# Kernel tuning notes

Measured on AMD Instinct MI355X. Metric: run time of the kernel, lower is better.

The kernel has to match this reference:

```python
import jax, jax.numpy as jnp
import numpy as np

B, N, D, H, E = 4, 4096, 1024, 16, 256
HD = D // H  # head_dim = 64


def setup_inputs() -> dict:
    key = jax.random.key(0)
    k1, k2, k3, k4, k5 = jax.random.split(key, 5)
    scale = 1.0 / np.sqrt(D)
    return {
        "x": jax.random.normal(k1, (B, N, D), dtype=jnp.float32),
        "proj_weight_all": jax.random.normal(k2, (N, E), dtype=jnp.float32) * (1.0 / np.sqrt(N)),
        "W_q": jax.random.normal(k3, (D, D), dtype=jnp.float32) * scale,
        "W_k": jax.random.normal(k4, (D, D), dtype=jnp.float32) * scale,
        "W_v": jax.random.normal(k5, (D, D), dtype=jnp.float32) * scale,
    }


def reference(x, proj_weight_all, W_q, W_k, W_v):
    # QKV projections: [B,N,D] @ [D,D] -> [B,N,D]
    q = jnp.einsum('bnd,de->bne', x, W_q)
    k = jnp.einsum('bnd,de->bne', x, W_k)
    v = jnp.einsum('bnd,de->bne', x, W_v)
    # split heads -> [B,H,N,hd]
    split = lambda t: t.reshape(B, N, H, HD).transpose(0, 2, 1, 3)
    qh, kh, vh = split(q), split(k), split(v)
    # low-rank sequence projection of K/V: [B,H,N,hd] x [N,E] -> [B,H,E,hd]
    k_proj = jnp.einsum('bhnd,ne->bhed', kh, proj_weight_all)
    v_proj = jnp.einsum('bhnd,ne->bhed', vh, proj_weight_all)
    # attention over projected length E (dropout p=0 -> identity)
    scores = jnp.einsum('bhnd,bhed->bhne', qh, k_proj) / jnp.sqrt(jnp.float32(HD))
    attn = jax.nn.softmax(scores, axis=-1)  # [B,H,N,E]
    out = jnp.einsum('bhne,bhed->bhnd', attn, v_proj)
    # concat heads -> [B,N,D]
    return out.transpose(0, 2, 1, 3).reshape(B, N, D)
```

## Files before the change

kernel.cpp:

```cpp
#include <hip/hip_runtime.h>
#include <hip/hip_bf16.h>

#define B_ 4
#define N_ 4096
#define D_ 1024
#define H_ 16
#define E_ 256
#define HD_ 64

typedef __attribute__((ext_vector_type(8))) short bf16x8;
typedef __attribute__((ext_vector_type(4))) short shortx4;
typedef __attribute__((ext_vector_type(4))) float floatx4;

__device__ inline short f2bf(float f) {
  __hip_bfloat16 h = __float2bfloat16(f);
  short s;
  __builtin_memcpy(&s, &h, 2);
  return s;
}

__device__ inline void gld_lds16(const short* g, short* l) {
  __builtin_amdgcn_global_load_lds(
      (const __attribute__((address_space(1))) void*)g,
      (__attribute__((address_space(3))) void*)l, 16, 0, 0);
}

template <bool CAST_COPY>
__device__ inline void transpose_body(const float* __restrict__ src,
                                      short* __restrict__ dstT,
                                      short* __restrict__ dstC,
                                      int R, int C) {
  __shared__ float tile[32][33];
  int c0 = blockIdx.x * 32;
  int r0 = blockIdx.y * 32;
  int tx = threadIdx.x;
  int ty = threadIdx.y;
#pragma unroll
  for (int i = 0; i < 4; ++i) {
    int r = ty * 4 + i;
    float v = src[(size_t)(r0 + r) * C + (c0 + tx)];
    tile[r][tx] = v;
    if constexpr (CAST_COPY)
      dstC[(size_t)(r0 + r) * C + (c0 + tx)] = f2bf(v);
  }
  __syncthreads();
#pragma unroll
  for (int i = 0; i < 4; ++i) {
    int c = ty * 4 + i;
    dstT[(size_t)(c0 + c) * R + (r0 + tx)] = f2bf(tile[tx][c]);
  }
}

__global__ void transpose_x_kernel(const float* __restrict__ x,
                                   short* __restrict__ xtb,
                                   short* __restrict__ xb) {
  int b = blockIdx.z;
  transpose_body<true>(x + (size_t)b * N_ * D_, xtb + (size_t)b * D_ * N_,
                       xb + (size_t)b * N_ * D_, N_, D_);
}

__global__ void transpose_w_kernel(const float* __restrict__ Wq,
                                   const float* __restrict__ Wk,
                                   const float* __restrict__ Wv,
                                   short* __restrict__ WqT,
                                   short* __restrict__ WkT,
                                   short* __restrict__ WvT) {
  int z = blockIdx.z;
  const float* src = (z == 0) ? Wq : (z == 1) ? Wk : Wv;
  short* dst = (z == 0) ? WqT : (z == 1) ? WkT : WvT;
  transpose_body<false>(src, dst, nullptr, D_, D_);
}

__global__ void transpose_p_kernel(const float* __restrict__ proj,
                                   short* __restrict__ projT) {
  transpose_body<false>(proj, projT, nullptr, N_, E_);
}

__global__ void cast_f32_bf16_kernel(const float* __restrict__ in,
                                     short* __restrict__ out) {
  int i = (blockIdx.x * 256 + threadIdx.x) * 4;
  const float4 v = *(const float4*)(in + i);
  shortx4 o;
  o[0] = f2bf(v.x); o[1] = f2bf(v.y); o[2] = f2bf(v.z); o[3] = f2bf(v.w);
  *(shortx4*)(out + i) = o;
}

__device__ inline bf16x8 frag256(const short* slab, int row, int q) {
  int a = (row << 6) + (q << 4);
  a ^= ((a >> 7) & 7) << 4;
  return *(const bf16x8*)(slab + (a >> 1));
}

#define G_BAR() __builtin_amdgcn_s_barrier()
#define G_LGK0() asm volatile("s_waitcnt lgkmcnt(0)" ::: "memory")
#define G_VM6() asm volatile("s_waitcnt vmcnt(6)" ::: "memory")
#define G_VM0() asm volatile("s_waitcnt vmcnt(0)" ::: "memory")
#define G_PRIO1() __builtin_amdgcn_s_setprio(1)
#define G_PRIO0() __builtin_amdgcn_s_setprio(0)

__global__ __launch_bounds__(512) void gemm256_bt_kernel(
    const short* __restrict__ Ag, const short* __restrict__ Btg,
    short* __restrict__ Cg, int M, int Nc, int K) {
  __shared__ short lds[65536];
#define SLAB(b, o, kk2) (lds + ((((((b) << 1) | (o)) << 1) | (kk2)) * 8192))

  int tid = threadIdx.x;
  int lane = tid & 63;
  int w = tid >> 6;
  int l16 = lane & 15;
  int quad = lane >> 4;
  int wm = w >> 2;
  int wn = w & 3;

  int nwg = gridDim.x;
  int cpx = nwg >> 3;
  int bid = blockIdx.x;
  int swz = (bid & 7) * cpx + (bid >> 3);
  int ntile_m = M >> 8;
  int tm = swz % ntile_m;
  int tn = swz / ntile_m;
  int m0 = tm * 256, n0 = tn * 256;

  const short* gA = Ag + (size_t)m0 * K;
  const short* gB = Btg + (size_t)n0 * K;

  int a0 = tid * 16;
  int w0 = a0 ^ (((a0 >> 7) & 7) << 4);
  int a1 = (tid + 512) * 16;
  int w1 = a1 ^ (((a1 >> 7) & 7) << 4);
  size_t so0 = (size_t)(w0 >> 6) * K + ((w0 & 63) >> 1);
  size_t so1 = (size_t)(w1 >> 6) * K + ((w1 & 63) >> 1);

#define STAGE(b, o, kk2, gsrc)                      \
  do {                                              \
    short* _sl = SLAB(b, o, kk2);                   \
    gld_lds16((gsrc) + so0, _sl + tid * 8);         \
    gld_lds16((gsrc) + so1, _sl + 4096 + tid * 8);  \
  } while (0)

  floatx4 acc[8][4];
#pragma unroll
  for (int i = 0; i < 8; ++i)
#pragma unroll
    for (int j = 0; j < 4; ++j) acc[i][j] = (floatx4){0.f, 0.f, 0.f, 0.f};

  bf16x8 af[8], bfr0, bfr1;

#define READ_A(bu, kk2)                                             \
  do {                                                              \
    const short* _sa = SLAB(bu, 0, kk2);                            \
    _Pragma("unroll") for (int mt = 0; mt < 8; ++mt)                \
        af[mt] = frag256(_sa, wm * 128 + mt * 16 + l16, quad);      \
  } while (0)
#define READ_B(bu, kk2, ntb)                                        \
  do {                                                              \
    const short* _sb = SLAB(bu, 1, kk2);                            \
    bfr0 = frag256(_sb, wn * 64 + (ntb)*16 + l16, quad);            \
    bfr1 = frag256(_sb, wn * 64 + (ntb)*16 + 16 + l16, quad);       \
  } while (0)
#define MFMA2(c0, c1)                                                          \
  do {                                                                         \
    _Pragma("unroll") for (int mt = 0; mt < 8; ++mt) {                         \
      acc[mt][c0] =                                                            \
          __builtin_amdgcn_mfma_f32_16x16x32_bf16(af[mt], bfr0, acc[mt][c0],   \
                                                  0, 0, 0);                    \
      acc[mt][c1] =                                                            \
          __builtin_amdgcn_mfma_f32_16x16x32_bf16(af[mt], bfr1, acc[mt][c1],   \
                                                  0, 0, 0);                    \
    }                                                                          \
  } while (0)

  STAGE(0, 0, 0, gA);
  STAGE(0, 1, 0, gB);
  STAGE(0, 0, 1, gA + 32);
  STAGE(0, 1, 1, gB + 32);
  STAGE(1, 0, 0, gA + 64);
  STAGE(1, 1, 0, gB + 64);
  STAGE(1, 0, 1, gA + 96);
  G_VM6();
  G_BAR();

  const int NI = K >> 7;
#pragma unroll 1
  for (int it = 0; it < NI - 1; ++it) {
    int t0 = it * 2;
    const short* gAt2 = gA + (t0 + 2) * 64;
    const short* gBt2 = gB + (t0 + 2) * 64;
    const short* gAt3 = gA + (t0 + 3) * 64;
    const short* gBt3 = gB + (t0 + 3) * 64;
    READ_A(0, 0); READ_B(0, 0, 0);
    STAGE(1, 1, 1, gB + (t0 + 1) * 64 + 32);
    G_BAR(); G_LGK0(); G_PRIO1(); MFMA2(0, 1); G_PRIO0(); G_BAR();
    READ_B(0, 0, 2);
    STAGE(0, 0, 0, gAt2);
    G_BAR(); G_LGK0(); G_PRIO1(); MFMA2(2, 3); G_PRIO0(); G_BAR();
    READ_A(0, 1); READ_B(0, 1, 0);
    STAGE(0, 1, 0, gBt2);
    G_BAR(); G_LGK0(); G_PRIO1(); MFMA2(0, 1); G_PRIO0(); G_BAR();
    READ_B(0, 1, 2);
    STAGE(0, 0, 1, gAt2 + 32);
    G_BAR(); G_LGK0(); G_PRIO1(); MFMA2(2, 3); G_PRIO0(); G_VM6(); G_BAR();
    READ_A(1, 0); READ_B(1, 0, 0);
    STAGE(0, 1, 1, gBt2 + 32);
    G_BAR(); G_LGK0(); G_PRIO1(); MFMA2(0, 1); G_PRIO0(); G_BAR();
    READ_B(1, 0, 2);
    STAGE(1, 0, 0, gAt3);
    G_BAR(); G_LGK0(); G_PRIO1(); MFMA2(2, 3); G_PRIO0(); G_BAR();
    READ_A(1, 1); READ_B(1, 1, 0);
    STAGE(1, 1, 0, gBt3);
    G_BAR(); G_LGK0(); G_PRIO1(); MFMA2(0, 1); G_PRIO0(); G_BAR();
    READ_B(1, 1, 2);
    STAGE(1, 0, 1, gAt3 + 32);
    G_BAR(); G_LGK0(); G_PRIO1(); MFMA2(2, 3); G_PRIO0(); G_VM6(); G_BAR();
  }

  {
    int t0 = (NI - 1) * 2;
    READ_A(0, 0); READ_B(0, 0, 0);
    STAGE(1, 1, 1, gB + (t0 + 1) * 64 + 32);
    G_BAR(); G_LGK0(); G_PRIO1(); MFMA2(0, 1); G_PRIO0(); G_BAR();
    READ_B(0, 0, 2);
    G_BAR(); G_LGK0(); G_PRIO1(); MFMA2(2, 3); G_PRIO0(); G_BAR();
    READ_A(0, 1); READ_B(0, 1, 0);
    G_BAR(); G_LGK0(); G_PRIO1(); MFMA2(0, 1); G_PRIO0(); G_BAR();
    READ_B(0, 1, 2);
    G_BAR(); G_LGK0(); G_PRIO1(); MFMA2(2, 3); G_PRIO0(); G_VM0(); G_BAR();
    READ_A(1, 0); READ_B(1, 0, 0);
    G_BAR(); G_LGK0(); G_PRIO1(); MFMA2(0, 1); G_PRIO0(); G_BAR();
    READ_B(1, 0, 2);
    G_BAR(); G_LGK0(); G_PRIO1(); MFMA2(2, 3); G_PRIO0(); G_BAR();
    READ_A(1, 1); READ_B(1, 1, 0);
    G_BAR(); G_LGK0(); G_PRIO1(); MFMA2(0, 1); G_PRIO0(); G_BAR();
    READ_B(1, 1, 2);
    G_BAR(); G_LGK0(); G_PRIO1(); MFMA2(2, 3); G_PRIO0();
  }

#pragma unroll
  for (int mt = 0; mt < 8; ++mt)
#pragma unroll
    for (int nt = 0; nt < 4; ++nt)
#pragma unroll
      for (int r = 0; r < 4; ++r) {
        size_t row = (size_t)(m0 + wm * 128 + mt * 16 + quad * 4 + r);
        size_t col = (size_t)(n0 + wn * 64 + nt * 16 + l16);
        Cg[row * Nc + col] = f2bf(acc[mt][nt][r]);
      }
#undef SLAB
#undef STAGE
#undef READ_A
#undef READ_B
#undef MFMA2
}

__global__ __launch_bounds__(256) void gemm128_splitk_kernel(
    const short* __restrict__ Ag, const short* __restrict__ Btg,
    float* __restrict__ Cfg, int M, int Nc, int K, int KS,
    long sA, long sB, long sC) {
  __shared__ short lds_a[128 * 32];
  __shared__ short lds_b[128 * 32];
  int tid = threadIdx.x;
  int lane = tid & 63;
  int w = tid >> 6;
  int l16 = lane & 15;
  int quad = lane >> 4;
  int wm = w >> 1, wn = w & 1;
  int m0 = blockIdx.x * 128, n0 = blockIdx.y * 128;
  int bz = blockIdx.z / KS;
  int ks = blockIdx.z % KS;
  int kchunk = K / KS;
  int k0 = ks * kchunk;

  const short* A = Ag + (size_t)bz * sA;
  const short* Bt = Btg + (size_t)bz * sB;
  float* Cf = Cfg + (size_t)bz * sC;

  int srow = tid >> 2;
  int skcol = (tid & 3) * 8;
  const short* ag = A + (size_t)(m0 + srow) * K + skcol;
  const short* bg = Bt + (size_t)(n0 + srow) * K + skcol;
  short* la = lds_a + tid * 8;
  short* lb = lds_b + tid * 8;
  const size_t half = (size_t)64 * K;

  floatx4 acc[4][4];
#pragma unroll
  for (int i = 0; i < 4; ++i)
#pragma unroll
    for (int j = 0; j < 4; ++j) acc[i][j] = (floatx4){0.f, 0.f, 0.f, 0.f};

  for (int k = k0; k < k0 + kchunk; k += 32) {
    gld_lds16(ag + k, la);
    gld_lds16(ag + half + k, la + 64 * 32);
    gld_lds16(bg + k, lb);
    gld_lds16(bg + half + k, lb + 64 * 32);
    __syncthreads();

    bf16x8 af[4], bf[4];
#pragma unroll
    for (int mt = 0; mt < 4; ++mt)
      af[mt] = *(const bf16x8*)(lds_a + (wm * 64 + mt * 16 + l16) * 32 + quad * 8);
#pragma unroll
    for (int nt = 0; nt < 4; ++nt)
      bf[nt] = *(const bf16x8*)(lds_b + (wn * 64 + nt * 16 + l16) * 32 + quad * 8);
#pragma unroll
    for (int mt = 0; mt < 4; ++mt)
#pragma unroll
      for (int nt = 0; nt < 4; ++nt)
        acc[mt][nt] = __builtin_amdgcn_mfma_f32_16x16x32_bf16(af[mt], bf[nt], acc[mt][nt], 0, 0, 0);
    __syncthreads();
  }

#pragma unroll
  for (int mt = 0; mt < 4; ++mt)
#pragma unroll
    for (int nt = 0; nt < 4; ++nt)
#pragma unroll
      for (int r = 0; r < 4; ++r) {
        size_t row = (size_t)(m0 + wm * 64 + mt * 16 + quad * 4 + r);
        size_t col = (size_t)(n0 + wn * 64 + nt * 16 + l16);
        atomicAdd(&Cf[row * Nc + col], acc[mt][nt][r]);
      }
}

__global__ __launch_bounds__(256) void gemm_kv_kernel(
    const short* __restrict__ xp, const short* __restrict__ WkT,
    const short* __restrict__ WvT, short* __restrict__ kpb,
    short* __restrict__ vpT) {
  int tid = threadIdx.x;
  int w = tid >> 6;
  int lane = tid & 63;
  int l16 = lane & 15;
  int quad = lane >> 4;
  int m_base = blockIdx.x * 64 + (w >> 1) * 32;
  int n_base = blockIdx.y * 64 + (w & 1) * 32;
  int b = blockIdx.z;

  const short* Ab = xp + (size_t)b * E_ * D_;
  short* Ck = kpb + (size_t)b * E_ * D_;
  short* Cv = vpT + (size_t)b * D_ * E_;

  floatx4 acck[2][2], accv[2][2];
#pragma unroll
  for (int i = 0; i < 2; ++i)
#pragma unroll
    for (int j = 0; j < 2; ++j) {
      acck[i][j] = (floatx4){0.f, 0.f, 0.f, 0.f};
      accv[i][j] = (floatx4){0.f, 0.f, 0.f, 0.f};
    }

  for (int k = 0; k < D_; k += 32) {
    bf16x8 a[2], bk[2], bv[2];
#pragma unroll
    for (int mt = 0; mt < 2; ++mt)
      a[mt] = *(const bf16x8*)(Ab + (size_t)(m_base + mt * 16 + l16) * D_ + k + quad * 8);
#pragma unroll
    for (int nt = 0; nt < 2; ++nt) {
      size_t off = (size_t)(n_base + nt * 16 + l16) * D_ + k + quad * 8;
      bk[nt] = *(const bf16x8*)(WkT + off);
      bv[nt] = *(const bf16x8*)(WvT + off);
    }
#pragma unroll
    for (int mt = 0; mt < 2; ++mt)
#pragma unroll
      for (int nt = 0; nt < 2; ++nt) {
        acck[mt][nt] = __builtin_amdgcn_mfma_f32_16x16x32_bf16(a[mt], bk[nt], acck[mt][nt], 0, 0, 0);
        accv[mt][nt] = __builtin_amdgcn_mfma_f32_16x16x32_bf16(a[mt], bv[nt], accv[mt][nt], 0, 0, 0);
      }
  }

#pragma unroll
  for (int mt = 0; mt < 2; ++mt)
#pragma unroll
    for (int nt = 0; nt < 2; ++nt)
#pragma unroll
      for (int r = 0; r < 4; ++r) {
        size_t row = (size_t)(m_base + mt * 16 + quad * 4 + r);
        size_t col = (size_t)(n_base + nt * 16 + l16);
        Ck[row * D_ + col] = f2bf(acck[mt][nt][r]);
        Cv[col * E_ + row] = f2bf(accv[mt][nt][r]);
      }
}

__global__ __launch_bounds__(512) void attn_kernel(
    const short* __restrict__ q,
    const short* __restrict__ kp,
    const short* __restrict__ vpT,
    float* __restrict__ out) {
  __shared__ short lds_kp_p[17408];
  __shared__ short lds_vp[16384];

  int tid = threadIdx.x;
  int w = tid >> 6;
  int lane = tid & 63;
  int l16 = lane & 15;
  int quad = lane >> 4;
  int n0 = blockIdx.x * 128;
  int h = blockIdx.y;
  int b = blockIdx.z;

  {
    const short* kpg = kp + (size_t)b * E_ * D_ + h * 64;
    int r0 = tid >> 3;
    int sseg = (tid & 7) ^ (r0 & 7);
#pragma unroll
    for (int j = 0; j < 4; ++j)
      gld_lds16(kpg + (size_t)(r0 + j * 64) * D_ + sseg * 8,
                lds_kp_p + j * 4096 + tid * 8);
  }
  {
    const short* vpg = vpT + (size_t)b * D_ * E_ + (size_t)(h * 64) * E_;
    int s1 = tid & 31;
    int rb = tid >> 5;
    int sseg = (s1 & 24) | ((s1 & 7) ^ (rb & 7));
#pragma unroll
    for (int j = 0; j < 4; ++j)
      gld_lds16(vpg + (size_t)(rb + j * 16) * E_ + sseg * 8,
                lds_vp + j * 4096 + tid * 8);
  }

  const short* qbase = q + ((size_t)(b * N_ + n0 + w * 16 + l16)) * D_ + h * 64;
  bf16x8 qf0 = *(const bf16x8*)(qbase + quad * 8);
  bf16x8 qf1 = *(const bf16x8*)(qbase + 32 + quad * 8);

  __syncthreads();

  floatx4 s[16];
#pragma unroll
  for (int t = 0; t < 16; ++t) s[t] = (floatx4){0.f, 0.f, 0.f, 0.f};

  int sw = l16 & 7;
#pragma unroll
  for (int t = 0; t < 16; ++t) {
    int r = t * 16 + l16;
    const short* rowp = lds_kp_p + r * 64;
    bf16x8 a0 = *(const bf16x8*)(rowp + ((quad) ^ sw) * 8);
    bf16x8 a1 = *(const bf16x8*)(rowp + ((4 + quad) ^ sw) * 8);
    s[t] = __builtin_amdgcn_mfma_f32_16x16x32_bf16(a0, qf0, s[t], 0, 0, 0);
    s[t] = __builtin_amdgcn_mfma_f32_16x16x32_bf16(a1, qf1, s[t], 0, 0, 0);
  }

  float mx = -1e30f;
#pragma unroll
  for (int t = 0; t < 16; ++t)
#pragma unroll
    for (int r = 0; r < 4; ++r) {
      s[t][r] *= 0.125f;
      mx = fmaxf(mx, s[t][r]);
    }
  mx = fmaxf(mx, __shfl_xor(mx, 16, 64));
  mx = fmaxf(mx, __shfl_xor(mx, 32, 64));

  float lsum = 0.f;
#pragma unroll
  for (int t = 0; t < 16; ++t)
#pragma unroll
    for (int r = 0; r < 4; ++r) {
      s[t][r] = __expf(s[t][r] - mx);
      lsum += s[t][r];
    }
  lsum += __shfl_xor(lsum, 16, 64);
  lsum += __shfl_xor(lsum, 32, 64);

  __syncthreads();

  short* pbase = lds_kp_p + w * 2176;
  floatx4 o4[4];
#pragma unroll
  for (int t2 = 0; t2 < 4; ++t2) o4[t2] = (floatx4){0.f, 0.f, 0.f, 0.f};

#pragma unroll
  for (int hf = 0; hf < 2; ++hf) {
#pragma unroll
    for (int t = 0; t < 8; ++t)
#pragma unroll
      for (int r = 0; r < 4; ++r)
        pbase[l16 * 136 + t * 16 + quad * 4 + r] = f2bf(s[hf * 8 + t][r]);

#pragma unroll
    for (int es2 = 0; es2 < 4; ++es2) {
      bf16x8 pa = *(const bf16x8*)(pbase + l16 * 136 + es2 * 32 + quad * 8);
      int es = hf * 4 + es2;
#pragma unroll
      for (int t2 = 0; t2 < 4; ++t2) {
        int rr = t2 * 16 + l16;
        int seg = es * 4 + quad;
        int sg = (seg & 24) | ((seg & 7) ^ sw);
        bf16x8 vf = *(const bf16x8*)(lds_vp + rr * 256 + sg * 8);
        o4[t2] = __builtin_amdgcn_mfma_f32_16x16x32_bf16(pa, vf, o4[t2], 0, 0, 0);
      }
    }
  }

  float linv[4];
#pragma unroll
  for (int r = 0; r < 4; ++r)
    linv[r] = 1.0f / __shfl(lsum, (lane & 48) | (quad * 4 + r), 64);

#pragma unroll
  for (int r = 0; r < 4; ++r) {
    int n = n0 + w * 16 + quad * 4 + r;
#pragma unroll
    for (int t2 = 0; t2 < 4; ++t2)
      out[((size_t)(b * N_ + n)) * D_ + h * 64 + t2 * 16 + l16] = o4[t2][r] * linv[r];
  }
}

extern "C" void kernel_launch(void* const* d_in, const int* in_sizes, int n_in,
                              void* d_out, int out_size, void* d_ws, size_t ws_size,
                              hipStream_t stream) {
  const float* x    = (const float*)d_in[0];
  const float* proj = (const float*)d_in[1];
  const float* Wq   = (const float*)d_in[2];
  const float* Wk   = (const float*)d_in[3];
  const float* Wv   = (const float*)d_in[4];
  float* out = (float*)d_out;

  short* p = (short*)d_ws;
  short* xtb_qb = p; p += (size_t)B_ * D_ * N_;
  short* xb     = p; p += (size_t)B_ * N_ * D_;
  short* WqT    = p; p += (size_t)D_ * D_;
  short* WkT    = p; p += (size_t)D_ * D_;
  short* WvT    = p; p += (size_t)D_ * D_;
  short* projT  = p; p += (size_t)E_ * N_;
  short* xp     = p; p += (size_t)B_ * E_ * D_;
  short* kpb    = p; p += (size_t)B_ * E_ * D_;
  short* vpT    = p; p += (size_t)B_ * D_ * E_;
  float* xp_f32 = (float*)p;
  short* xtb = xtb_qb;
  short* qb  = xtb_qb;

  dim3 blkT(32, 8);
  transpose_x_kernel<<<dim3(D_ / 32, N_ / 32, B_), blkT, 0, stream>>>(x, xtb, xb);
  transpose_w_kernel<<<dim3(D_ / 32, D_ / 32, 3), blkT, 0, stream>>>(Wq, Wk, Wv, WqT, WkT, WvT);
  transpose_p_kernel<<<dim3(E_ / 32, N_ / 32, 1), blkT, 0, stream>>>(proj, projT);

  hipMemsetAsync(xp_f32, 0, (size_t)B_ * E_ * D_ * sizeof(float), stream);
  const int KS = 8;
  gemm128_splitk_kernel<<<dim3(E_ / 128, D_ / 128, B_ * KS), 256, 0, stream>>>(
      projT, xtb, xp_f32, E_, D_, N_, KS, 0, (long)D_ * N_, (long)E_ * D_);
  cast_f32_bf16_kernel<<<(B_ * E_ * D_) / 1024, 256, 0, stream>>>(xp_f32, xp);

  gemm256_bt_kernel<<<dim3(((B_ * N_) / 256) * (D_ / 256)), 512, 0, stream>>>(
      xb, WqT, qb, B_ * N_, D_, D_);

  gemm_kv_kernel<<<dim3(E_ / 64, D_ / 64, B_), 256, 0, stream>>>(
      xp, WkT, WvT, kpb, vpT);

  attn_kernel<<<dim3(N_ / 128, H_, B_), 512, 0, stream>>>(qb, kpb, vpT, out);
}
```

Baseline: 285.6 us.

## Replace split-K xp GEMM with single-pass 4-stage pipelined 64x64 tile kernel

Replaces the split-K GEMM (memset, fp32 atomics, then a separate cast kernel) for the x-projection with one kernel that computes 64x64 output tiles over the full K=4096. It uses a 4-deep global-to-LDS pipeline with swizzled LDS and explicit vmcnt waits, plus XCD-aware block mapping, and writes bf16 directly. This removes the atomics, the memset and the cast launch. The trade-off is that each block now walks a long K loop, and only 256 blocks are launched.

```diff
diff --git a/kernel.cpp b/kernel.cpp
--- a/kernel.cpp
+++ b/kernel.cpp
@@ -24,6 +24,16 @@
       (const __attribute__((address_space(1))) void*)g,
       (__attribute__((address_space(3))) void*)l, 16, 0, 0);
 }
+
+#define G_BAR() __builtin_amdgcn_s_barrier()
+#define G_LGK0() asm volatile("s_waitcnt lgkmcnt(0)" ::: "memory")
+#define G_VM0() asm volatile("s_waitcnt vmcnt(0)" ::: "memory")
+#define G_VM4() asm volatile("s_waitcnt vmcnt(4)" ::: "memory")
+#define G_VM6() asm volatile("s_waitcnt vmcnt(6)" ::: "memory")
+#define G_VM8() asm volatile("s_waitcnt vmcnt(8)" ::: "memory")
+#define G_VM12() asm volatile("s_waitcnt vmcnt(12)" ::: "memory")
+#define G_PRIO1() __builtin_amdgcn_s_setprio(1)
+#define G_PRIO0() __builtin_amdgcn_s_setprio(0)
 
 template <bool CAST_COPY>
 __device__ inline void transpose_body(const float* __restrict__ src,
@@ -76,13 +86,118 @@
   transpose_body<false>(proj, projT, nullptr, N_, E_);
 }
 
-__global__ void cast_f32_bf16_kernel(const float* __restrict__ in,
-                                     short* __restrict__ out) {
-  int i = (blockIdx.x * 256 + threadIdx.x) * 4;
-  const float4 v = *(const float4*)(in + i);
-  shortx4 o;
-  o[0] = f2bf(v.x); o[1] = f2bf(v.y); o[2] = f2bf(v.z); o[3] = f2bf(v.w);
-  *(shortx4*)(out + i) = o;
+__device__ inline bf16x8 fragx(const short* slab, int row, int q) {
+  int a = (row << 7) + (q << 4);
+  a ^= ((a >> 7) & 7) << 4;
+  return *(const bf16x8*)(slab + (a >> 1));
+}
+
+__global__ __launch_bounds__(256) void xp_kernel(
+    const short* __restrict__ projT, const short* __restrict__ xtb,
+    short* __restrict__ xp) {
+  __shared__ short lds[32768];
+#define XSLAB(bu, o) (lds + (((bu) << 1) | (o)) * 4096)
+
+  int tid = threadIdx.x;
+  int lane = tid & 63;
+  int w = tid >> 6;
+  int l16 = lane & 15;
+  int quad = lane >> 4;
+  int wm = w >> 1, wn = w & 1;
+
+  int bid = blockIdx.x;
+  int xcd = bid & 7;
+  int slot = bid >> 3;
+  int et = slot & 3;
+  int grp = (slot >> 2) * 8 + xcd;
+  int b = grp >> 4;
+  int dt = grp & 15;
+  int e0 = et * 64, d0 = dt * 64;
+
+  const short* Abase = projT + (size_t)e0 * N_;
+  const short* Bbase = xtb + (size_t)b * D_ * N_ + (size_t)d0 * N_;
+
+  int p0 = tid * 16;
+  int w0s = p0 ^ (((p0 >> 7) & 7) << 4);
+  int p1 = p0 + 4096;
+  int w1s = p1 ^ (((p1 >> 7) & 7) << 4);
+  size_t so0 = (size_t)(w0s >> 7) * N_ + ((w0s & 127) >> 1);
+  size_t so1 = (size_t)(w1s >> 7) * N_ + ((w1s & 127) >> 1);
+
+#define XSTAGE(bu, k)                                      \
+  do {                                                     \
+    short* _la = XSLAB(bu, 0);                             \
+    short* _lb = XSLAB(bu, 1);                             \
+    gld_lds16(Abase + (k) + so0, _la + tid * 8);           \
+    gld_lds16(Abase + (k) + so1, _la + 2048 + tid * 8);    \
+    gld_lds16(Bbase + (k) + so0, _lb + tid * 8);           \
+    gld_lds16(Bbase + (k) + so1, _lb + 2048 + tid * 8);    \
+  } while (0)
+
+  floatx4 acc[2][2];
+#pragma unroll
+  for (int i = 0; i < 2; ++i)
+#pragma unroll
+    for (int j = 0; j < 2; ++j) acc[i][j] = (floatx4){0.f, 0.f, 0.f, 0.f};
+
+  bf16x8 afr[2][2], bfr[2][2];
+
+#define XREAD(bu)                                                          \
+  do {                                                                     \
+    const short* _sa = XSLAB(bu, 0);                                       \
+    const short* _sb = XSLAB(bu, 1);                                       \
+    _Pragma("unroll") for (int kk = 0; kk < 2; ++kk) {                     \
+      _Pragma("unroll") for (int mt = 0; mt < 2; ++mt)                     \
+          afr[kk][mt] = fragx(_sa, wm * 32 + mt * 16 + l16, kk * 4 + quad);\
+      _Pragma("unroll") for (int nt = 0; nt < 2; ++nt)                     \
+          bfr[kk][nt] = fragx(_sb, wn * 32 + nt * 16 + l16, kk * 4 + quad);\
+    }                                                                      \
+  } while (0)
+
+#define XMFMA()                                                            \
+  do {                                                                     \
+    _Pragma("unroll") for (int kk = 0; kk < 2; ++kk)                       \
+      _Pragma("unroll") for (int mt = 0; mt < 2; ++mt)                     \
+        _Pragma("unroll") for (int nt = 0; nt < 2; ++nt)                   \
+            acc[mt][nt] = __builtin_amdgcn_mfma_f32_16x16x32_bf16(         \
+                afr[kk][mt], bfr[kk][nt], acc[mt][nt], 0, 0, 0);           \
+  } while (0)
+
+  XSTAGE(0, 0);
+  XSTAGE(1, 64);
+  XSTAGE(2, 128);
+  XSTAGE(3, 192);
+
+#pragma unroll 1
+  for (int t = 0; t < (N_ / 64) - 4; ++t) {
+    G_VM12();
+    G_BAR();
+    XREAD(t & 3);
+    G_LGK0();
+    G_BAR();
+    XSTAGE(t & 3, (t + 4) * 64);
+    G_PRIO1(); XMFMA(); G_PRIO0();
+  }
+  G_VM12(); G_BAR(); XREAD(0); G_LGK0(); G_PRIO1(); XMFMA(); G_PRIO0();
+  G_VM8();  G_BAR(); XREAD(1); G_LGK0(); G_PRIO1(); XMFMA(); G_PRIO0();
+  G_VM4();  G_BAR(); XREAD(2); G_LGK0(); G_PRIO1(); XMFMA(); G_PRIO0();
+  G_VM0();  G_BAR(); XREAD(3); G_LGK0(); G_PRIO1(); XMFMA(); G_PRIO0();
+
+  short* C = xp + (size_t)b * E_ * D_;
+#pragma unroll
+  for (int mt = 0; mt < 2; ++mt)
+#pragma unroll
+    for (int nt = 0; nt < 2; ++nt)
+#pragma unroll
+      for (int r = 0; r < 4; ++r) {
+        size_t row = (size_t)(e0 + wm * 32 + mt * 16 + quad * 4 + r);
+        size_t col = (size_t)(d0 + wn * 32 + nt * 16 + l16);
+        C[row * D_ + col] = f2bf(acc[mt][nt][r]);
+      }
+#undef XSLAB
+#undef XSTAGE
+#undef XREAD
+#undef XMFMA
 }
 
 __device__ inline bf16x8 frag256(const short* slab, int row, int q) {
@@ -90,13 +205,6 @@
   a ^= ((a >> 7) & 7) << 4;
   return *(const bf16x8*)(slab + (a >> 1));
 }
-
-#define G_BAR() __builtin_amdgcn_s_barrier()
-#define G_LGK0() asm volatile("s_waitcnt lgkmcnt(0)" ::: "memory")
-#define G_VM6() asm volatile("s_waitcnt vmcnt(6)" ::: "memory")
-#define G_VM0() asm volatile("s_waitcnt vmcnt(0)" ::: "memory")
-#define G_PRIO1() __builtin_amdgcn_s_setprio(1)
-#define G_PRIO0() __builtin_amdgcn_s_setprio(0)
 
 __global__ __launch_bounds__(512) void gemm256_bt_kernel(
     const short* __restrict__ Ag, const short* __restrict__ Btg,
@@ -250,76 +358,6 @@
 #undef READ_A
 #undef READ_B
 #undef MFMA2
-}
-
-__global__ __launch_bounds__(256) void gemm128_splitk_kernel(
-    const short* __restrict__ Ag, const short* __restrict__ Btg,
-    float* __restrict__ Cfg, int M, int Nc, int K, int KS,
-    long sA, long sB, long sC) {
-  __shared__ short lds_a[128 * 32];
-  __shared__ short lds_b[128 * 32];
-  int tid = threadIdx.x;
-  int lane = tid & 63;
-  int w = tid >> 6;
-  int l16 = lane & 15;
-  int quad = lane >> 4;
-  int wm = w >> 1, wn = w & 1;
-  int m0 = blockIdx.x * 128, n0 = blockIdx.y * 128;
-  int bz = blockIdx.z / KS;
-  int ks = blockIdx.z % KS;
-  int kchunk = K / KS;
-  int k0 = ks * kchunk;
-
-  const short* A = Ag + (size_t)bz * sA;
-  const short* Bt = Btg + (size_t)bz * sB;
-  float* Cf = Cfg + (size_t)bz * sC;
-
-  int srow = tid >> 2;
-  int skcol = (tid & 3) * 8;
-  const short* ag = A + (size_t)(m0 + srow) * K + skcol;
-  const short* bg = Bt + (size_t)(n0 + srow) * K + skcol;
-  short* la = lds_a + tid * 8;
-  short* lb = lds_b + tid * 8;
-  const size_t half = (size_t)64 * K;
-
-  floatx4 acc[4][4];
-#pragma unroll
-  for (int i = 0; i < 4; ++i)
-#pragma unroll
-    for (int j = 0; j < 4; ++j) acc[i][j] = (floatx4){0.f, 0.f, 0.f, 0.f};
-
-  for (int k = k0; k < k0 + kchunk; k += 32) {
-    gld_lds16(ag + k, la);
-    gld_lds16(ag + half + k, la + 64 * 32);
-    gld_lds16(bg + k, lb);
-    gld_lds16(bg + half + k, lb + 64 * 32);
-    __syncthreads();
-
-    bf16x8 af[4], bf[4];
-#pragma unroll
-    for (int mt = 0; mt < 4; ++mt)
-      af[mt] = *(const bf16x8*)(lds_a + (wm * 64 + mt * 16 + l16) * 32 + quad * 8);
-#pragma unroll
-    for (int nt = 0; nt < 4; ++nt)
-      bf[nt] = *(const bf16x8*)(lds_b + (wn * 64 + nt * 16 + l16) * 32 + quad * 8);
-#pragma unroll
-    for (int mt = 0; mt < 4; ++mt)
-#pragma unroll
-      for (int nt = 0; nt < 4; ++nt)
-        acc[mt][nt] = __builtin_amdgcn_mfma_f32_16x16x32_bf16(af[mt], bf[nt], acc[mt][nt], 0, 0, 0);
-    __syncthreads();
-  }
-
-#pragma unroll
-  for (int mt = 0; mt < 4; ++mt)
-#pragma unroll
-    for (int nt = 0; nt < 4; ++nt)
-#pragma unroll
-      for (int r = 0; r < 4; ++r) {
-        size_t row = (size_t)(m0 + wm * 64 + mt * 16 + quad * 4 + r);
-        size_t col = (size_t)(n0 + wn * 64 + nt * 16 + l16);
-        atomicAdd(&Cf[row * Nc + col], acc[mt][nt][r]);
-      }
 }
 
 __global__ __launch_bounds__(256) void gemm_kv_kernel(
@@ -525,7 +563,6 @@
   short* xp     = p; p += (size_t)B_ * E_ * D_;
   short* kpb    = p; p += (size_t)B_ * E_ * D_;
   short* vpT    = p; p += (size_t)B_ * D_ * E_;
-  float* xp_f32 = (float*)p;
   short* xtb = xtb_qb;
   short* qb  = xtb_qb;
 
@@ -534,11 +571,7 @@
   transpose_w_kernel<<<dim3(D_ / 32, D_ / 32, 3), blkT, 0, stream>>>(Wq, Wk, Wv, WqT, WkT, WvT);
   transpose_p_kernel<<<dim3(E_ / 32, N_ / 32, 1), blkT, 0, stream>>>(proj, projT);
 
-  hipMemsetAsync(xp_f32, 0, (size_t)B_ * E_ * D_ * sizeof(float), stream);
-  const int KS = 8;
-  gemm128_splitk_kernel<<<dim3(E_ / 128, D_ / 128, B_ * KS), 256, 0, stream>>>(
-      projT, xtb, xp_f32, E_, D_, N_, KS, 0, (long)D_ * N_, (long)E_ * D_);
-  cast_f32_bf16_kernel<<<(B_ * E_ * D_) / 1024, 256, 0, stream>>>(xp_f32, xp);
+  xp_kernel<<<256, 256, 0, stream>>>(projT, xtb, xp);
 
   gemm256_bt_kernel<<<dim3(((B_ * N_) / 256) * (D_ / 256)), 512, 0, stream>>>(
       xb, WqT, qb, B_ * N_, D_, D_);
```

After: 253.4 us. -11.3%, faster.

## Replace split-K atomic xp GEMM with in-block K reduction and vectorize transposes

Applied to the files above, without the earlier changes.

Replaces the memset, the split-K GEMM with fp32 atomics and the separate bf16 cast kernel with one xp_kernel. In that kernel 8 waves each cover a K slice, reading operands straight from global memory, then sum their partials through LDS and write bf16 directly. This removes two launches, the fp32 scratch buffer and the atomic traffic. The transpose kernels also move to 1D 256-thread blocks using float4 loads and shortx4 stores. The trade-off is that xp_kernel skips LDS staging, so global loads are uncoalesced per lane and each block needs a large LDS reduction buffer, which may limit occupancy.

```diff
diff --git a/kernel.cpp b/kernel.cpp
--- a/kernel.cpp
+++ b/kernel.cpp
@@ -24,6 +24,13 @@
       (const __attribute__((address_space(1))) void*)g,
       (__attribute__((address_space(3))) void*)l, 16, 0, 0);
 }
+
+#define G_BAR() __builtin_amdgcn_s_barrier()
+#define G_LGK0() asm volatile("s_waitcnt lgkmcnt(0)" ::: "memory")
+#define G_VM0() asm volatile("s_waitcnt vmcnt(0)" ::: "memory")
+#define G_VM6() asm volatile("s_waitcnt vmcnt(6)" ::: "memory")
+#define G_PRIO1() __builtin_amdgcn_s_setprio(1)
+#define G_PRIO0() __builtin_amdgcn_s_setprio(0)
 
 template <bool CAST_COPY>
 __device__ inline void transpose_body(const float* __restrict__ src,
@@ -33,56 +40,130 @@
   __shared__ float tile[32][33];
   int c0 = blockIdx.x * 32;
   int r0 = blockIdx.y * 32;
-  int tx = threadIdx.x;
-  int ty = threadIdx.y;
-#pragma unroll
-  for (int i = 0; i < 4; ++i) {
-    int r = ty * 4 + i;
-    float v = src[(size_t)(r0 + r) * C + (c0 + tx)];
-    tile[r][tx] = v;
-    if constexpr (CAST_COPY)
-      dstC[(size_t)(r0 + r) * C + (c0 + tx)] = f2bf(v);
+  int tid = threadIdx.x;
+  {
+    int r = tid >> 3;
+    int c4 = (tid & 7) * 4;
+    float4 v = *(const float4*)(src + (size_t)(r0 + r) * C + (c0 + c4));
+    tile[r][c4 + 0] = v.x;
+    tile[r][c4 + 1] = v.y;
+    tile[r][c4 + 2] = v.z;
+    tile[r][c4 + 3] = v.w;
+    if constexpr (CAST_COPY) {
+      shortx4 o;
+      o[0] = f2bf(v.x); o[1] = f2bf(v.y); o[2] = f2bf(v.z); o[3] = f2bf(v.w);
+      *(shortx4*)(dstC + (size_t)(r0 + r) * C + (c0 + c4)) = o;
+    }
   }
   __syncthreads();
-#pragma unroll
-  for (int i = 0; i < 4; ++i) {
-    int c = ty * 4 + i;
-    dstT[(size_t)(c0 + c) * R + (r0 + tx)] = f2bf(tile[tx][c]);
-  }
-}
-
-__global__ void transpose_x_kernel(const float* __restrict__ x,
-                                   short* __restrict__ xtb,
-                                   short* __restrict__ xb) {
+  {
+    int c = tid >> 3;
+    int r4 = (tid & 7) * 4;
+    shortx4 o;
+#pragma unroll
+    for (int i = 0; i < 4; ++i) o[i] = f2bf(tile[r4 + i][c]);
+    *(shortx4*)(dstT + (size_t)(c0 + c) * R + (r0 + r4)) = o;
+  }
+}
+
+__global__ __launch_bounds__(256) void transpose_x_kernel(
+    const float* __restrict__ x, short* __restrict__ xtb,
+    short* __restrict__ xb) {
   int b = blockIdx.z;
   transpose_body<true>(x + (size_t)b * N_ * D_, xtb + (size_t)b * D_ * N_,
                        xb + (size_t)b * N_ * D_, N_, D_);
 }
 
-__global__ void transpose_w_kernel(const float* __restrict__ Wq,
-                                   const float* __restrict__ Wk,
-                                   const float* __restrict__ Wv,
-                                   short* __restrict__ WqT,
-                                   short* __restrict__ WkT,
-                                   short* __restrict__ WvT) {
+__global__ __launch_bounds__(256) void transpose_w_kernel(
+    const float* __restrict__ Wq, const float* __restrict__ Wk,
+    const float* __restrict__ Wv, short* __restrict__ WqT,
+    short* __restrict__ WkT, short* __restrict__ WvT) {
   int z = blockIdx.z;
   const float* src = (z == 0) ? Wq : (z == 1) ? Wk : Wv;
   short* dst = (z == 0) ? WqT : (z == 1) ? WkT : WvT;
   transpose_body<false>(src, dst, nullptr, D_, D_);
 }
 
-__global__ void transpose_p_kernel(const float* __restrict__ proj,
-                                   short* __restrict__ projT) {
+__global__ __launch_bounds__(256) void transpose_p_kernel(
+    const float* __restrict__ proj, short* __restrict__ projT) {
   transpose_body<false>(proj, projT, nullptr, N_, E_);
 }
 
-__global__ void cast_f32_bf16_kernel(const float* __restrict__ in,
-                                     short* __restrict__ out) {
-  int i = (blockIdx.x * 256 + threadIdx.x) * 4;
-  const float4 v = *(const float4*)(in + i);
-  shortx4 o;
-  o[0] = f2bf(v.x); o[1] = f2bf(v.y); o[2] = f2bf(v.z); o[3] = f2bf(v.w);
-  *(shortx4*)(out + i) = o;
+__global__ __launch_bounds__(512) void xp_kernel(
+    const short* __restrict__ projT, const short* __restrict__ xtb,
+    short* __restrict__ xp) {
+  __shared__ float red[8][64][72];
+
+  int tid = threadIdx.x;
+  int lane = tid & 63;
+  int w = tid >> 6;
+  int l16 = lane & 15;
+  int quad = lane >> 4;
+
+  int bid = blockIdx.x;
+  int xcd = bid & 7;
+  int slot = bid >> 3;
+  int et = slot & 3;
+  int grp = (slot >> 2) * 8 + xcd;
+  int b = grp >> 4;
+  int dt = grp & 15;
+  int e0 = et * 64, d0 = dt * 64;
+
+  const short* A = projT + (size_t)e0 * N_;
+  const short* Bt = xtb + (size_t)b * D_ * N_ + (size_t)d0 * N_;
+
+  floatx4 acc[4][4];
+#pragma unroll
+  for (int i = 0; i < 4; ++i)
+#pragma unroll
+    for (int j = 0; j < 4; ++j) acc[i][j] = (floatx4){0.f, 0.f, 0.f, 0.f};
+
+  int k0 = w * 512;
+#pragma unroll 2
+  for (int i = 0; i < 16; ++i) {
+    int k = k0 + i * 32;
+    bf16x8 a[4], bb[4];
+#pragma unroll
+    for (int mt = 0; mt < 4; ++mt)
+      a[mt] = *(const bf16x8*)(A + (size_t)(mt * 16 + l16) * N_ + k + quad * 8);
+#pragma unroll
+    for (int nt = 0; nt < 4; ++nt)
+      bb[nt] = *(const bf16x8*)(Bt + (size_t)(nt * 16 + l16) * N_ + k + quad * 8);
+#pragma unroll
+    for (int mt = 0; mt < 4; ++mt)
+#pragma unroll
+      for (int nt = 0; nt < 4; ++nt)
+        acc[mt][nt] = __builtin_amdgcn_mfma_f32_16x16x32_bf16(
+            a[mt], bb[nt], acc[mt][nt], 0, 0, 0);
+  }
+
+#pragma unroll
+  for (int mt = 0; mt < 4; ++mt)
+#pragma unroll
+    for (int nt = 0; nt < 4; ++nt)
+#pragma unroll
+      for (int r = 0; r < 4; ++r)
+        red[w][mt * 16 + quad * 4 + r][nt * 16 + l16] = acc[mt][nt][r];
+  __syncthreads();
+
+  {
+    int row = tid >> 3;
+    int c8 = (tid & 7) * 8;
+    float s[8];
+#pragma unroll
+    for (int j = 0; j < 8; ++j) s[j] = 0.f;
+#pragma unroll
+    for (int w8 = 0; w8 < 8; ++w8) {
+      const float4 v0 = *(const float4*)&red[w8][row][c8];
+      const float4 v1 = *(const float4*)&red[w8][row][c8 + 4];
+      s[0] += v0.x; s[1] += v0.y; s[2] += v0.z; s[3] += v0.w;
+      s[4] += v1.x; s[5] += v1.y; s[6] += v1.z; s[7] += v1.w;
+    }
+    bf16x8 o;
+#pragma unroll
+    for (int j = 0; j < 8; ++j) o[j] = f2bf(s[j]);
+    *(bf16x8*)(xp + (size_t)b * E_ * D_ + (size_t)(e0 + row) * D_ + d0 + c8) = o;
+  }
 }
 
 __device__ inline bf16x8 frag256(const short* slab, int row, int q) {
@@ -90,13 +171,6 @@
   a ^= ((a >> 7) & 7) << 4;
   return *(const bf16x8*)(slab + (a >> 1));
 }
-
-#define G_BAR() __builtin_amdgcn_s_barrier()
-#define G_LGK0() asm volatile("s_waitcnt lgkmcnt(0)" ::: "memory")
-#define G_VM6() asm volatile("s_waitcnt vmcnt(6)" ::: "memory")
-#define G_VM0() asm volatile("s_waitcnt vmcnt(0)" ::: "memory")
-#define G_PRIO1() __builtin_amdgcn_s_setprio(1)
-#define G_PRIO0() __builtin_amdgcn_s_setprio(0)
 
 __global__ __launch_bounds__(512) void gemm256_bt_kernel(
     const short* __restrict__ Ag, const short* __restrict__ Btg,
@@ -252,76 +326,6 @@
 #undef MFMA2
 }
 
-__global__ __launch_bounds__(256) void gemm128_splitk_kernel(
-    const short* __restrict__ Ag, const short* __restrict__ Btg,
-    float* __restrict__ Cfg, int M, int Nc, int K, int KS,
-    long sA, long sB, long sC) {
-  __shared__ short lds_a[128 * 32];
-  __shared__ short lds_b[128 * 32];
-  int tid = threadIdx.x;
-  int lane = tid & 63;
-  int w = tid >> 6;
-  int l16 = lane & 15;
-  int quad = lane >> 4;
-  int wm = w >> 1, wn = w & 1;
-  int m0 = blockIdx.x * 128, n0 = blockIdx.y * 128;
-  int bz = blockIdx.z / KS;
-  int ks = blockIdx.z % KS;
-  int kchunk = K / KS;
-  int k0 = ks * kchunk;
-
-  const short* A = Ag + (size_t)bz * sA;
-  const short* Bt = Btg + (size_t)bz * sB;
-  float* Cf = Cfg + (size_t)bz * sC;
-
-  int srow = tid >> 2;
-  int skcol = (tid & 3) * 8;
-  const short* ag = A + (size_t)(m0 + srow) * K + skcol;
-  const short* bg = Bt + (size_t)(n0 + srow) * K + skcol;
-  short* la = lds_a + tid * 8;
-  short* lb = lds_b + tid * 8;
-  const size_t half = (size_t)64 * K;
-
-  floatx4 acc[4][4];
-#pragma unroll
-  for (int i = 0; i < 4; ++i)
-#pragma unroll
-    for (int j = 0; j < 4; ++j) acc[i][j] = (floatx4){0.f, 0.f, 0.f, 0.f};
-
-  for (int k = k0; k < k0 + kchunk; k += 32) {
-    gld_lds16(ag + k, la);
-    gld_lds16(ag + half + k, la + 64 * 32);
-    gld_lds16(bg + k, lb);
-    gld_lds16(bg + half + k, lb + 64 * 32);
-    __syncthreads();
-
-    bf16x8 af[4], bf[4];
-#pragma unroll
-    for (int mt = 0; mt < 4; ++mt)
-      af[mt] = *(const bf16x8*)(lds_a + (wm * 64 + mt * 16 + l16) * 32 + quad * 8);
-#pragma unroll
-    for (int nt = 0; nt < 4; ++nt)
-      bf[nt] = *(const bf16x8*)(lds_b + (wn * 64 + nt * 16 + l16) * 32 + quad * 8);
-#pragma unroll
-    for (int mt = 0; mt < 4; ++mt)
-#pragma unroll
-      for (int nt = 0; nt < 4; ++nt)
-        acc[mt][nt] = __builtin_amdgcn_mfma_f32_16x16x32_bf16(af[mt], bf[nt], acc[mt][nt], 0, 0, 0);
-    __syncthreads();
-  }
-
-#pragma unroll
-  for (int mt = 0; mt < 4; ++mt)
-#pragma unroll
-    for (int nt = 0; nt < 4; ++nt)
-#pragma unroll
-      for (int r = 0; r < 4; ++r) {
-        size_t row = (size_t)(m0 + wm * 64 + mt * 16 + quad * 4 + r);
-        size_t col = (size_t)(n0 + wn * 64 + nt * 16 + l16);
-        atomicAdd(&Cf[row * Nc + col], acc[mt][nt][r]);
-      }
-}
-
 __global__ __launch_bounds__(256) void gemm_kv_kernel(
     const short* __restrict__ xp, const short* __restrict__ WkT,
     const short* __restrict__ WvT, short* __restrict__ kpb,
@@ -525,20 +529,14 @@
   short* xp     = p; p += (size_t)B_ * E_ * D_;
   short* kpb    = p; p += (size_t)B_ * E_ * D_;
   short* vpT    = p; p += (size_t)B_ * D_ * E_;
-  float* xp_f32 = (float*)p;
   short* xtb = xtb_qb;
   short* qb  = xtb_qb;
 
-  dim3 blkT(32, 8);
-  transpose_x_kernel<<<dim3(D_ / 32, N_ / 32, B_), blkT, 0, stream>>>(x, xtb, xb);
-  transpose_w_kernel<<<dim3(D_ / 32, D_ / 32, 3), blkT, 0, stream>>>(Wq, Wk, Wv, WqT, WkT, WvT);
-  transpose_p_kernel<<<dim3(E_ / 32, N_ / 32, 1), blkT, 0, stream>>>(proj, projT);
-
-  hipMemsetAsync(xp_f32, 0, (size_t)B_ * E_ * D_ * sizeof(float), stream);
-  const int KS = 8;
-  gemm128_splitk_kernel<<<dim3(E_ / 128, D_ / 128, B_ * KS), 256, 0, stream>>>(
-      projT, xtb, xp_f32, E_, D_, N_, KS, 0, (long)D_ * N_, (long)E_ * D_);
-  cast_f32_bf16_kernel<<<(B_ * E_ * D_) / 1024, 256, 0, stream>>>(xp_f32, xp);
+  transpose_x_kernel<<<dim3(D_ / 32, N_ / 32, B_), 256, 0, stream>>>(x, xtb, xb);
+  transpose_w_kernel<<<dim3(D_ / 32, D_ / 32, 3), 256, 0, stream>>>(Wq, Wk, Wv, WqT, WkT, WvT);
+  transpose_p_kernel<<<dim3(E_ / 32, N_ / 32, 1), 256, 0, stream>>>(proj, projT);
+
+  xp_kernel<<<256, 512, 0, stream>>>(projT, xtb, xp);
 
   gemm256_bt_kernel<<<dim3(((B_ * N_) / 256) * (D_ / 256)), 512, 0, stream>>>(
       xb, WqT, qb, B_ * N_, D_, D_);
```

After: 266.2 us. 6.8% less time.
